# Performance work log

Measured on AMD Instinct MI355X. Metric: run time of the kernel, lower is better.

The kernel has to match this reference:

```python
import jax, jax.numpy as jnp
import numpy as np

B, L, D, NH, NV, T = 4096, 5, 128, 16, 4, 100
NUM_USERS = NUM_ITEMS = 100000
FC1_DIM = NV * D + NH * sum(L - l + 1 for l in range(1, L + 1))  # 752


def setup_inputs() -> dict:
    key = jax.random.key(0)
    ks = jax.random.split(key, 12)
    s = 0.02
    return {
        "seq": jax.random.randint(ks[0], (B, L), 0, NUM_ITEMS),
        "user": jax.random.randint(ks[1], (B,), 0, NUM_USERS),
        "items": jax.random.randint(ks[2], (B, T), 0, NUM_ITEMS),
        "item_table": jax.random.normal(ks[3], (NUM_ITEMS, D), jnp.float32) * s,
        "user_table": jax.random.normal(ks[4], (NUM_USERS, D), jnp.float32) * s,
        "Wv": jax.random.normal(ks[5], (NV, L), jnp.float32) * s,
        "bv": jnp.zeros((NV,), jnp.float32),
        "Wh": jax.random.normal(ks[6], (L, NH, L, D), jnp.float32) * s,
        "bh": jnp.zeros((L, NH), jnp.float32),
        "W1": jax.random.normal(ks[7], (FC1_DIM, D), jnp.float32) * s,
        "b1": jnp.zeros((D,), jnp.float32),
        "W2_table": jax.random.normal(ks[8], (NUM_ITEMS, 2 * D), jnp.float32) * s,
        "b2_table": jnp.zeros((NUM_ITEMS, 1), jnp.float32),
        "_predict": 1,
    }


def reference(seq, user, items, item_table, user_table, Wv, bv, Wh, bh, W1, b1, W2_table, b2_table, _predict):
    emb = item_table[seq]            # (B, L, D)
    uemb = user_table[user]          # (B, D)

    # vertical conv: kernel (L,1), nv out channels -> (B, NV, D), flattened
    ver = jnp.einsum("btd,vt->bvd", emb, Wv) + bv[None, :, None]
    ver_flat = ver.reshape(B, NV * D)

    # horizontal convs: for each kernel length l, NH filters of shape (l, D)
    hor = []
    for l in range(1, L + 1):
        lout = L - l + 1
        # windows: (B, lout, l, D) built from l shifted views
        win = jnp.stack([emb[:, s:s + lout] for s in range(l)], axis=2)
        h = jnp.einsum("btsd,fsd->bft", win, Wh[l - 1, :, :l]) + bh[l - 1][None, :, None]
        hor.append(jax.nn.relu(h).reshape(B, NH * lout))

    z = jnp.concatenate([ver_flat] + hor, axis=1)      # (B, FC1_DIM)
    x = jax.nn.relu(z @ W1 + b1)                        # (B, D)
    xc = jnp.concatenate([x, uemb], axis=1)             # (B, 2D)

    w2 = W2_table[items]                                # (B, T, 2D)
    b2 = b2_table[items][..., 0]                        # (B, T)
    res = jnp.einsum("btd,bd->bt", w2, xc) + b2
    return res
```

## Files before the change

### kernel.cpp

```cpp
#include <hip/hip_runtime.h>


constexpr int Bsz  = 4096;
constexpr int Lq   = 5;
constexpr int Dd   = 128;
constexpr int NHh  = 16;
constexpr int NVv  = 4;
constexpr int Tt   = 100;
constexpr int FC1  = 752;
constexpr int G    = 4;
constexpr int NTHR = 256;

__global__ __launch_bounds__(NTHR, 4) void caser_front(
    const int* __restrict__ seq, const int* __restrict__ user,
    const float* __restrict__ item_table, const float* __restrict__ user_table,
    const float* __restrict__ Wv, const float* __restrict__ bv,
    const float* __restrict__ Wh, const float* __restrict__ bh,
    const float* __restrict__ W1, const float* __restrict__ b1,
    float* __restrict__ xc_ws)
{
    __shared__ float emb[G][Lq * Dd];
    __shared__ float z[G][FC1];
    __shared__ float xc[G][2 * Dd];

    const int tid = threadIdx.x;
    const int b0  = blockIdx.x * G;

    for (int idx = tid; idx < G * Lq * Dd; idx += NTHR) {
        int gt  = idx >> 7;
        int d   = idx & (Dd - 1);
        int row = seq[b0 * Lq + gt];
        emb[0][idx] = item_table[row * Dd + d];
    }
    for (int idx = tid; idx < G * Dd; idx += NTHR) {
        int g = idx >> 7, d = idx & (Dd - 1);
        xc[g][Dd + d] = user_table[user[b0 + g] * Dd + d];
    }
    __syncthreads();

    for (int idx = tid; idx < G * NVv * Dd; idx += NTHR) {
        int g = idx >> 9;
        int v = (idx >> 7) & 3;
        int d = idx & (Dd - 1);
        float acc = bv[v];
        #pragma unroll
        for (int t = 0; t < Lq; ++t)
            acc = fmaf(emb[g][t * Dd + d], Wv[v * Lq + t], acc);
        z[g][v * Dd + d] = acc;
    }

    if (tid < 240) {
        int glt = tid >> 4, f = tid & 15;
        int l, t;
        if      (glt < 5)  { l = 1; t = glt; }
        else if (glt < 9)  { l = 2; t = glt - 5; }
        else if (glt < 12) { l = 3; t = glt - 9; }
        else if (glt < 14) { l = 4; t = glt - 12; }
        else               { l = 5; t = 0; }
        const int lout = Lq - l + 1;
        const int zoff = (l == 1) ? 0 : (l == 2) ? 80 : (l == 3) ? 144
                       : (l == 4) ? 192 : 224;
        float acc[G];
        {
            float bias = bh[(l - 1) * NHh + f];
            #pragma unroll
            for (int g = 0; g < G; ++g) acc[g] = bias;
        }
        for (int s = 0; s < l; ++s) {
            const float4* w4 = reinterpret_cast<const float4*>(
                Wh + (((l - 1) * NHh + f) * Lq + s) * Dd);
            const int ebase = (t + s) * Dd;
            #pragma unroll 4
            for (int d4 = 0; d4 < Dd / 4; ++d4) {
                float4 w = w4[d4];
                #pragma unroll
                for (int g = 0; g < G; ++g) {
                    float4 e = *reinterpret_cast<const float4*>(
                        &emb[g][ebase + d4 * 4]);
                    acc[g] = fmaf(e.x, w.x,
                             fmaf(e.y, w.y,
                             fmaf(e.z, w.z,
                             fmaf(e.w, w.w, acc[g]))));
                }
            }
        }
        #pragma unroll
        for (int g = 0; g < G; ++g)
            z[g][NVv * Dd + zoff + f * lout + t] = fmaxf(acc[g], 0.0f);
    }
    __syncthreads();

    float* part = &emb[0][0];
    {
        int j = tid & (Dd - 1);
        int half = tid >> 7;
        float acc[G] = {0.f, 0.f, 0.f, 0.f};
        const float* w1p = W1 + j;
        int i0 = half * (FC1 / 2);
        for (int i = i0; i < i0 + FC1 / 2; i += 4) {
            float4 zz[G];
            #pragma unroll
            for (int g = 0; g < G; ++g)
                zz[g] = *reinterpret_cast<const float4*>(&z[g][i]);
            float w0 = w1p[(i + 0) * Dd];
            float w1 = w1p[(i + 1) * Dd];
            float w2 = w1p[(i + 2) * Dd];
            float w3 = w1p[(i + 3) * Dd];
            #pragma unroll
            for (int g = 0; g < G; ++g)
                acc[g] = fmaf(zz[g].x, w0,
                         fmaf(zz[g].y, w1,
                         fmaf(zz[g].z, w2,
                         fmaf(zz[g].w, w3, acc[g]))));
        }
        #pragma unroll
        for (int g = 0; g < G; ++g)
            part[(half * G + g) * Dd + j] = acc[g];
    }
    __syncthreads();
    if (tid < Dd) {
        #pragma unroll
        for (int g = 0; g < G; ++g)
            xc[g][tid] = fmaxf(part[g * Dd + tid] + part[(G + g) * Dd + tid]
                               + b1[tid], 0.0f);
    }
    __syncthreads();

    for (int idx = tid; idx < G * 2 * Dd; idx += NTHR)
        xc_ws[b0 * 2 * Dd + idx] = xc[0][idx];
}

__global__ __launch_bounds__(NTHR, 8) void caser_tail(
    const int* __restrict__ items,
    const float* __restrict__ W2_table, const float* __restrict__ b2_table,
    const float* __restrict__ xc_ws, float* __restrict__ out)
{
    __shared__ int   s_items[Tt];
    __shared__ float s_b2[Tt];

    const int b    = blockIdx.x;
    const int tid  = threadIdx.x;
    const int lane = tid & 63;
    const int wv   = tid >> 6;

    if (tid < Tt) {
        int it = items[b * Tt + tid];
        s_items[tid] = it;
        s_b2[tid]    = b2_table[it];
    }
    const float4 xf =
        reinterpret_cast<const float4*>(xc_ws + b * 2 * Dd)[lane];
    __syncthreads();

    #pragma unroll 4
    for (int k = 0; k < Tt / 4; ++k) {
        const int t = wv + k * 4;
        const float4* wp = reinterpret_cast<const float4*>(
            W2_table + (size_t)s_items[t] * (2 * Dd));
        float4 w = wp[lane];
        float v = fmaf(w.x, xf.x,
                  fmaf(w.y, xf.y,
                  fmaf(w.z, xf.z, w.w * xf.w)));
        #pragma unroll
        for (int off = 32; off; off >>= 1)
            v += __shfl_xor(v, off);
        if (lane == 0) out[b * Tt + t] = v + s_b2[t];
    }
}

extern "C" void kernel_launch(void* const* d_in, const int* in_sizes, int n_in,
                              void* d_out, int out_size, void* d_ws, size_t ws_size,
                              hipStream_t stream) {
    const int*   seq        = (const int*)  d_in[0];
    const int*   user       = (const int*)  d_in[1];
    const int*   items      = (const int*)  d_in[2];
    const float* item_table = (const float*)d_in[3];
    const float* user_table = (const float*)d_in[4];
    const float* Wv         = (const float*)d_in[5];
    const float* bv         = (const float*)d_in[6];
    const float* Wh         = (const float*)d_in[7];
    const float* bh         = (const float*)d_in[8];
    const float* W1         = (const float*)d_in[9];
    const float* b1         = (const float*)d_in[10];
    const float* W2_table   = (const float*)d_in[11];
    const float* b2_table   = (const float*)d_in[12];
    float* out   = (float*)d_out;
    float* xc_ws = (float*)d_ws;

    caser_front<<<dim3(Bsz / G), dim3(NTHR), 0, stream>>>(
        seq, user, item_table, user_table, Wv, bv, Wh, bh, W1, b1, xc_ws);
    caser_tail<<<dim3(Bsz), dim3(NTHR), 0, stream>>>(
        items, W2_table, b2_table, xc_ws, out);
}
```

Before: 325.6 us.

## Pad embedding rows, prefetch conv/FC1 weights, split FC1 into four K-quarters

Pads the shared embedding rows from 128 to 132 floats so the horizontal-conv float4 reads hit fewer LDS bank conflicts. The horizontal conv now runs as one flattened loop that loads the next Wh float4 one step ahead. FC1 is rebuilt so each thread computes two output columns over a quarter of K, with software-prefetched float2 W1 loads and a four-way partial sum at the end. The tail kernel's launch-bounds occupancy hint and unroll factor are also retuned, which may change register allocation and occupancy.

```diff
diff --git a/kernel.cpp b/kernel.cpp
--- a/kernel.cpp
+++ b/kernel.cpp
@@ -4,10 +4,12 @@
 constexpr int Bsz  = 4096;
 constexpr int Lq   = 5;
 constexpr int Dd   = 128;
+constexpr int EP   = 132;
 constexpr int NHh  = 16;
 constexpr int NVv  = 4;
 constexpr int Tt   = 100;
 constexpr int FC1  = 752;
+constexpr int KQ   = FC1 / 4;
 constexpr int G    = 4;
 constexpr int NTHR = 256;
 
@@ -19,18 +21,19 @@
     const float* __restrict__ W1, const float* __restrict__ b1,
     float* __restrict__ xc_ws)
 {
-    __shared__ float emb[G][Lq * Dd];
+    __shared__ float emb[G][Lq * EP];
     __shared__ float z[G][FC1];
     __shared__ float xc[G][2 * Dd];
 
     const int tid = threadIdx.x;
     const int b0  = blockIdx.x * G;
+    float* embf = &emb[0][0];
 
     for (int idx = tid; idx < G * Lq * Dd; idx += NTHR) {
         int gt  = idx >> 7;
         int d   = idx & (Dd - 1);
         int row = seq[b0 * Lq + gt];
-        emb[0][idx] = item_table[row * Dd + d];
+        embf[gt * EP + d] = item_table[row * Dd + d];
     }
     for (int idx = tid; idx < G * Dd; idx += NTHR) {
         int g = idx >> 7, d = idx & (Dd - 1);
@@ -45,7 +48,7 @@
         float acc = bv[v];
         #pragma unroll
         for (int t = 0; t < Lq; ++t)
-            acc = fmaf(emb[g][t * Dd + d], Wv[v * Lq + t], acc);
+            acc = fmaf(emb[g][t * EP + d], Wv[v * Lq + t], acc);
         z[g][v * Dd + d] = acc;
     }
 
@@ -66,23 +69,26 @@
             #pragma unroll
             for (int g = 0; g < G; ++g) acc[g] = bias;
         }
-        for (int s = 0; s < l; ++s) {
-            const float4* w4 = reinterpret_cast<const float4*>(
-                Wh + (((l - 1) * NHh + f) * Lq + s) * Dd);
-            const int ebase = (t + s) * Dd;
-            #pragma unroll 4
-            for (int d4 = 0; d4 < Dd / 4; ++d4) {
-                float4 w = w4[d4];
-                #pragma unroll
-                for (int g = 0; g < G; ++g) {
-                    float4 e = *reinterpret_cast<const float4*>(
-                        &emb[g][ebase + d4 * 4]);
-                    acc[g] = fmaf(e.x, w.x,
-                             fmaf(e.y, w.y,
-                             fmaf(e.z, w.z,
-                             fmaf(e.w, w.w, acc[g]))));
-                }
+        const float4* w4 = reinterpret_cast<const float4*>(
+            Wh + (((l - 1) * NHh + f) * Lq) * Dd);
+        float4 wc = w4[t == t ? 0 : 0];
+        wc = w4[0];
+        const int niter = l * 32;
+        for (int it = 0; it < niter; ++it) {
+            float4 wn = (it + 1 < niter) ? w4[it + 1] : wc;
+            const int s  = it >> 5;
+            const int d4 = it & 31;
+            const int ebase = (t + s) * EP + d4 * 4;
+            #pragma unroll
+            for (int g = 0; g < G; ++g) {
+                float4 e = *reinterpret_cast<const float4*>(
+                    &embf[g * Lq * EP + ebase]);
+                acc[g] = fmaf(e.x, wc.x,
+                         fmaf(e.y, wc.y,
+                         fmaf(e.z, wc.z,
+                         fmaf(e.w, wc.w, acc[g]))));
             }
+            wc = wn;
         }
         #pragma unroll
         for (int g = 0; g < G; ++g)
@@ -90,39 +96,61 @@
     }
     __syncthreads();
 
-    float* part = &emb[0][0];
+    float* part = &embf[0];
     {
-        int j = tid & (Dd - 1);
-        int half = tid >> 7;
-        float acc[G] = {0.f, 0.f, 0.f, 0.f};
-        const float* w1p = W1 + j;
-        int i0 = half * (FC1 / 2);
-        for (int i = i0; i < i0 + FC1 / 2; i += 4) {
-            float4 zz[G];
-            #pragma unroll
-            for (int g = 0; g < G; ++g)
-                zz[g] = *reinterpret_cast<const float4*>(&z[g][i]);
-            float w0 = w1p[(i + 0) * Dd];
-            float w1 = w1p[(i + 1) * Dd];
-            float w2 = w1p[(i + 2) * Dd];
-            float w3 = w1p[(i + 3) * Dd];
-            #pragma unroll
-            for (int g = 0; g < G; ++g)
-                acc[g] = fmaf(zz[g].x, w0,
-                         fmaf(zz[g].y, w1,
-                         fmaf(zz[g].z, w2,
-                         fmaf(zz[g].w, w3, acc[g]))));
+        const int q  = tid >> 6;
+        const int j2 = tid & 63;
+        const float* w1p = W1 + 2 * j2;
+        float2 acc[G];
+        #pragma unroll
+        for (int g = 0; g < G; ++g) acc[g] = make_float2(0.f, 0.f);
+        const int i0 = q * KQ;
+        float2 cw0, cw1, cw2, cw3, nw0, nw1, nw2, nw3;
+        cw0 = *reinterpret_cast<const float2*>(w1p + (i0 + 0) * Dd);
+        cw1 = *reinterpret_cast<const float2*>(w1p + (i0 + 1) * Dd);
+        cw2 = *reinterpret_cast<const float2*>(w1p + (i0 + 2) * Dd);
+        cw3 = *reinterpret_cast<const float2*>(w1p + (i0 + 3) * Dd);
+        for (int i = i0; i < i0 + KQ - 4; i += 4) {
+            nw0 = *reinterpret_cast<const float2*>(w1p + (i + 4) * Dd);
+            nw1 = *reinterpret_cast<const float2*>(w1p + (i + 5) * Dd);
+            nw2 = *reinterpret_cast<const float2*>(w1p + (i + 6) * Dd);
+            nw3 = *reinterpret_cast<const float2*>(w1p + (i + 7) * Dd);
+            #pragma unroll
+            for (int g = 0; g < G; ++g) {
+                float4 zz = *reinterpret_cast<const float4*>(&z[g][i]);
+                acc[g].x = fmaf(zz.w, cw3.x, fmaf(zz.z, cw2.x,
+                           fmaf(zz.y, cw1.x, fmaf(zz.x, cw0.x, acc[g].x))));
+                acc[g].y = fmaf(zz.w, cw3.y, fmaf(zz.z, cw2.y,
+                           fmaf(zz.y, cw1.y, fmaf(zz.x, cw0.y, acc[g].y))));
+            }
+            cw0 = nw0; cw1 = nw1; cw2 = nw2; cw3 = nw3;
+        }
+        {
+            const int i = i0 + KQ - 4;
+            #pragma unroll
+            for (int g = 0; g < G; ++g) {
+                float4 zz = *reinterpret_cast<const float4*>(&z[g][i]);
+                acc[g].x = fmaf(zz.w, cw3.x, fmaf(zz.z, cw2.x,
+                           fmaf(zz.y, cw1.x, fmaf(zz.x, cw0.x, acc[g].x))));
+                acc[g].y = fmaf(zz.w, cw3.y, fmaf(zz.z, cw2.y,
+                           fmaf(zz.y, cw1.y, fmaf(zz.x, cw0.y, acc[g].y))));
+            }
         }
         #pragma unroll
         for (int g = 0; g < G; ++g)
-            part[(half * G + g) * Dd + j] = acc[g];
+            *reinterpret_cast<float2*>(&part[(q * G + g) * Dd + 2 * j2])
+                = acc[g];
     }
     __syncthreads();
     if (tid < Dd) {
         #pragma unroll
-        for (int g = 0; g < G; ++g)
-            xc[g][tid] = fmaxf(part[g * Dd + tid] + part[(G + g) * Dd + tid]
-                               + b1[tid], 0.0f);
+        for (int g = 0; g < G; ++g) {
+            float s = part[g * Dd + tid]
+                    + part[(G + g) * Dd + tid]
+                    + part[(2 * G + g) * Dd + tid]
+                    + part[(3 * G + g) * Dd + tid];
+            xc[g][tid] = fmaxf(s + b1[tid], 0.0f);
+        }
     }
     __syncthreads();
 
@@ -130,7 +158,7 @@
         xc_ws[b0 * 2 * Dd + idx] = xc[0][idx];
 }
 
-__global__ __launch_bounds__(NTHR, 8) void caser_tail(
+__global__ __launch_bounds__(NTHR, 6) void caser_tail(
     const int* __restrict__ items,
     const float* __restrict__ W2_table, const float* __restrict__ b2_table,
     const float* __restrict__ xc_ws, float* __restrict__ out)
@@ -152,7 +180,7 @@
         reinterpret_cast<const float4*>(xc_ws + b * 2 * Dd)[lane];
     __syncthreads();
 
-    #pragma unroll 4
+    #pragma unroll 5
     for (int k = 0; k < Tt / 4; ++k) {
         const int t = wv + k * 4;
         const float4* wp = reinterpret_cast<const float4*>(
```

New measurement: 327.1 us. About the same (+0.5%).
